# Kernel tuning notes

Hardware: AMD Instinct MI355X
Metric: run time of the kernel (lower is better)

The kernel has to match this reference:

```python
import jax, jax.numpy as jnp
import numpy as np
import math

N = 1500; E = 24000; C_IN = 16; H = 64; NUM_LAYERS = 10; RATIO = 0.9
NEG = -1e9


def setup_inputs() -> dict:
    key = jax.random.key(0)
    ks = jax.random.split(key, 40)
    it = iter(range(40))
    def nrm(shape, scale=0.1):
        return jax.random.normal(ks[next(it)], shape, dtype=jnp.float32) * scale
    src = jax.random.randint(ks[next(it)], (E,), 0, N, dtype=jnp.int32)
    off = jax.random.randint(ks[next(it)], (E,), 1, N, dtype=jnp.int32)
    dst = (src + off) % N  # no self loops in the raw edge list
    return dict(
        x=nrm((N, C_IN), 1.0),
        edge_src=src, edge_dst=dst,
        W1=nrm((C_IN, H // 2)), b1=jnp.zeros((H // 2,), jnp.float32),
        W2=nrm((H // 2, H)), b2=jnp.zeros((H,), jnp.float32),
        W3=nrm((H, H)), b3=jnp.zeros((H,), jnp.float32),
        Wrel=nrm((NUM_LAYERS - 1, H, H)), brel=jnp.zeros((NUM_LAYERS - 1, H), jnp.float32),
        Wroot=nrm((NUM_LAYERS - 1, H, H)),
        pW=nrm((4, H, H)), pb=jnp.zeros((4, H), jnp.float32),
        leW1=nrm((4, H, 1)), leb1=jnp.zeros((4, 1), jnp.float32),
        leW2=nrm((4, H, 1)),
        leW3=nrm((4, H, 1)), leb3=jnp.zeros((4, 1), jnp.float32),
        linW1=nrm((NUM_LAYERS * H, H)), linb1=jnp.zeros((H,), jnp.float32),
        linW2=nrm((H, 10)), linb2=jnp.zeros((10,), jnp.float32),
    )


def _seg_mean(vals, idx, n):
    s = jax.ops.segment_sum(vals, idx, num_segments=n)
    c = jax.ops.segment_sum(jnp.ones((idx.shape[0],), vals.dtype), idx, num_segments=n)
    return s / jnp.maximum(c, 1.0)[:, None]


def _feast(x, W, b, srcL, dstL, n):
    # FeaStConv with heads=1: softmax over a single head == 1 -> mean of lin(x_j) + bias
    return _seg_mean((x @ W)[srcL], dstL, n) + b


def _gconv_sparse(x, src, dst, Wr, br, Wo, n):
    return _seg_mean(x[src], dst, n) @ Wr + br + x @ Wo


def _gconv_dense(x, A, Wr, br, Wo):
    # mean aggregation: divide weighted sum by count of (nonzero) in-edges
    Mf = (A != 0).astype(x.dtype)
    agg = (A.T @ x) / jnp.maximum(Mf.sum(0), 1.0)[:, None]
    return agg @ Wr + br + x @ Wo


def _topk_pool(xc, fitness, ratio):
    k = int(math.ceil(ratio * xc.shape[0]))
    fit_k, perm = jax.lax.top_k(fitness, k)
    return xc[perm] * fit_k[:, None], perm


def _asap_sparse(x, src, dst, pW, pb, leW1, leb1, leW2, leW3, leb3):
    n = x.shape[0]
    ar = jnp.arange(n, dtype=src.dtype)
    srcL = jnp.concatenate([src, ar])  # add remaining self loops (weight 1)
    dstL = jnp.concatenate([dst, ar])
    xq = jax.ops.segment_max(x[srcL], dstL, num_segments=n) @ pW + pb
    s = jax.nn.leaky_relu(jnp.sum(xq[dstL] * x[srcL], -1), 0.2)
    m = jax.ops.segment_max(s, dstL, num_segments=n)
    e = jnp.exp(s - m[dstL])
    score = e / jax.ops.segment_sum(e, dstL, num_segments=n)[dstL]
    xc = jax.ops.segment_sum(x[srcL] * score[:, None], dstL, num_segments=n)
    # LEConv fitness score (edge weight = 1)
    a = xc @ leW1 + leb1
    b = xc @ leW2
    agg = jax.ops.segment_sum(a[srcL] - b[dstL], dstL, num_segments=n)
    fitness = jax.nn.sigmoid((agg + xc @ leW3 + leb3)[:, 0])
    x_new, perm = _topk_pool(xc, fitness, RATIO)
    S = jnp.zeros((n, n), x.dtype).at[srcL, dstL].add(score)
    A = jnp.zeros((n, n), x.dtype).at[srcL, dstL].add(1.0)
    Sp = S[:, perm]
    A_new = Sp.T @ A @ Sp
    k = A_new.shape[0]
    return x_new, A_new * (1.0 - jnp.eye(k, dtype=x.dtype))  # remove diag


def _asap_dense(x, A, pW, pb, leW1, leb1, leW2, leW3, leb3):
    n = x.shape[0]
    A = A + jnp.diag((jnp.diag(A) == 0).astype(A.dtype))  # add remaining self loops
    M = A != 0
    Mf = M.astype(x.dtype)
    xq = jnp.max(jnp.where(M[:, :, None], x[:, None, :], NEG), axis=0) @ pW + pb  # [n,H]
    Sc = jnp.where(M, jax.nn.leaky_relu(x @ xq.T, 0.2), NEG)  # [j,i]
    m = Sc.max(0)
    e = jnp.where(M, jnp.exp(Sc - m), 0.0)
    score = e / e.sum(0)
    xc = score.T @ x
    a = xc @ leW1 + leb1
    b = xc @ leW2
    agg = Mf.T @ a - Mf.sum(0)[:, None] * b
    fitness = jax.nn.sigmoid((agg + xc @ leW3 + leb3)[:, 0])
    x_new, perm = _topk_pool(xc, fitness, RATIO)
    Sp = score[:, perm]
    A_new = Sp.T @ A @ Sp
    k = A_new.shape[0]
    return x_new, A_new * (1.0 - jnp.eye(k, dtype=x.dtype))


def _forward(x, edge_src, edge_dst, W1, b1, W2, b2, W3, b3, Wrel, brel, Wroot,
             pW, pb, leW1, leb1, leW2, leW3, leb3, linW1, linb1, linW2, linb2):
    n = x.shape[0]
    ar = jnp.arange(n, dtype=edge_src.dtype)
    srcL = jnp.concatenate([edge_src, ar])  # FeaStConv add_self_loops=True
    dstL = jnp.concatenate([edge_dst, ar])
    x = jax.nn.elu(_feast(x, W1, b1, srcL, dstL, n))
    x = jax.nn.elu(_feast(x, W2, b2, srcL, dstL, n))
    x = jax.nn.elu(_feast(x, W3, b3, srcL, dstL, n))
    xs = [x.mean(0, keepdims=True)]  # single graph -> global_mean_pool == mean
    A = None
    for i in range(NUM_LAYERS - 1):
        if A is None:
            x = jax.nn.relu(_gconv_sparse(x, edge_src, edge_dst, Wrel[i], brel[i], Wroot[i], x.shape[0]))
        else:
            x = jax.nn.relu(_gconv_dense(x, A, Wrel[i], brel[i], Wroot[i]))
        xs.append(x.mean(0, keepdims=True))
        if i % 2 == 0 and i < NUM_LAYERS - 2:
            p = i // 2
            args = (pW[p], pb[p], leW1[p], leb1[p], leW2[p], leW3[p], leb3[p])
            if A is None:
                x, A = _asap_sparse(x, edge_src, edge_dst, *args)
            else:
                x, A = _asap_dense(x, A, *args)
    h = jnp.concatenate(xs, axis=-1)  # [1, NUM_LAYERS*H] jumping-knowledge cat
    h = jax.nn.relu(h @ linW1 + linb1)
    return jax.nn.log_softmax(h @ linW2 + linb2, axis=-1)


def reference(x, edge_src, edge_dst, W1, b1, W2, b2, W3, b3, Wrel, brel, Wroot,
              pW, pb, leW1, leb1, leW2, leW3, leb3, linW1, linb1, linW2, linb2):
    return _forward(x, edge_src, edge_dst, W1, b1, W2, b2, W3, b3, Wrel, brel, Wroot,
                    pW, pb, leW1, leb1, leW2, leW3, leb3, linW1, linb1, linW2, linb2)
```

## Files before the change

### kernel.cpp

```cpp
#include <hip/hip_runtime.h>
#include <math.h>

#define NEGV -1000000000.0f

typedef short short8 __attribute__((ext_vector_type(8)));
typedef float floatx4 __attribute__((ext_vector_type(4)));

__device__ __forceinline__ float sigm(float x){ return 1.0f/(1.0f+expf(-x)); }
__device__ __forceinline__ void edge_sd(int e,const int* src,const int* dst,int E,int& s,int& d){
  if(e<E){ s=src[e]; d=dst[e]; } else { s=e-E; d=s; }
}
__device__ __forceinline__ ushort bf16rn(float x){
  unsigned u = __float_as_uint(x);
  unsigned r = (u + 0x7fffu + ((u>>16)&1u)) >> 16;
  return (ushort)r;
}
__device__ __forceinline__ float bf16f(ushort h){ return __uint_as_float(((unsigned)h)<<16); }

__global__ void k_zero(float* __restrict__ p, size_t n){
  size_t i = (size_t)blockIdx.x*256 + threadIdx.x;
  if (i < n) p[i] = 0.0f;
}
__global__ void k_fillm1(int* __restrict__ p, int n){
  int i = blockIdx.x*256 + threadIdx.x;
  if (i < n) p[i] = -1;
}
__global__ void k_ipos(const int* __restrict__ perm, int* __restrict__ ipos, int kk){
  int p = blockIdx.x*256 + threadIdx.x;
  if (p < kk) ipos[perm[p]] = p;
}
__global__ void k_prep2(const int* __restrict__ rowD,const int* __restrict__ eidD,
                        const float* __restrict__ scE,int2* __restrict__ Mt,int L2,int kk){
  int p = blockIdx.x*256+threadIdx.x; if(p>=L2) return;
  Mt[p] = make_int2(rowD[p]*kk, __float_as_int(scE[eidD[p]]));
}

__global__ void k_split3(const float* __restrict__ src,int R,int Cs,int ld,
                         ushort* __restrict__ dst,int Cp,int bmode){
  int idx = blockIdx.x*256+threadIdx.x;
  if (idx >= R*Cp) return;
  int r = idx / Cp, c = idx - r*Cp;
  float x = (c < Cs) ? src[(size_t)r*ld + c] : 0.0f;
  ushort h = bf16rn(x);
  ushort l = bf16rn(x - bf16f(h));
  size_t base = (size_t)r*(3*Cp) + c;
  dst[base]        = h;
  dst[base + Cp]   = bmode ? l : h;
  dst[base + 2*Cp] = bmode ? h : l;
}
__global__ void k_split3_Tdual(const float* __restrict__ src,int Rs,int Cs,int ld,
                               const int* __restrict__ gperm,const float* __restrict__ cscale,
                               const float* __restrict__ emax,
                               ushort* __restrict__ dstA,ushort* __restrict__ dstB,
                               ushort* __restrict__ dstCpad,int Kp){
  __shared__ float t[32][33];
  int tx = threadIdx.x & 31, ty = threadIdx.x >> 5;
  int kb = blockIdx.y*32, xb = blockIdx.x*32;
  int x = xb + tx;
  int gx = (x < Cs) ? gperm[x] : 0;
#pragma unroll
  for (int i=0;i<4;i++){
    int k = kb + ty + i*8;
    t[ty+i*8][tx] = (k < Rs && x < Cs) ? src[(size_t)k*ld + gx] : 0.0f;
  }
  __syncthreads();
  const int K3 = 3*Kp;
#pragma unroll
  for (int i=0;i<4;i++){
    int xo = xb + ty + i*8, ko = kb + tx;
    if (xo < Cs){
      float v = 0.0f;
      if (ko < Rs){
        int g = gperm[xo];
        v = expf(t[tx][ty+i*8] - emax[g]) * cscale[g];
      }
      ushort h = bf16rn(v);
      ushort l = bf16rn(v - bf16f(h));
      size_t base = (size_t)xo*K3 + ko;
      dstA[base] = h; dstA[base+Kp] = h; dstA[base+2*Kp] = l;
      dstB[base] = h; dstB[base+Kp] = l; dstB[base+2*Kp] = h;
      if (ko >= Rs){ dstCpad[base]=0; dstCpad[base+Kp]=0; dstCpad[base+2*Kp]=0; }
    }
  }
}

template<int EPI>
__global__ __launch_bounds__(256) void k_gemm_mfma(
    const ushort* __restrict__ A, const ushort* __restrict__ B,
    float* __restrict__ C, int ldc, int M, int N, int K3,
    const float* __restrict__ mask, int ldm)
{
  __shared__ ushort As[2][64][72];
  __shared__ ushort Bs[2][64][72];
  const int tid = threadIdx.x;
  const int m0 = blockIdx.y*64, n0 = blockIdx.x*64;
  const int w = tid>>6, lane = tid&63;
  const int lo4 = lane&15, quad = lane>>4;
  const int sr = tid>>2, sseg = tid&3;

  floatx4 acc[4];
#pragma unroll
  for(int c=0;c<4;c++){ acc[c][0]=0.f; acc[c][1]=0.f; acc[c][2]=0.f; acc[c][3]=0.f; }

  const size_t arow = (size_t)(m0+sr)*K3;
  const size_t brow = (size_t)(n0+sr)*K3;
  const bool aval = (m0+sr) < M;
  const bool bval = (n0+sr) < N;

  uint4 av0 = make_uint4(0,0,0,0), av1 = make_uint4(0,0,0,0);
  uint4 bv0 = make_uint4(0,0,0,0), bv1 = make_uint4(0,0,0,0);
  if (aval){ av0 = *(const uint4*)(A + arow + sseg*8);
             av1 = *(const uint4*)(A + arow + 32 + sseg*8); }
  if (bval){ bv0 = *(const uint4*)(B + brow + sseg*8);
             bv1 = *(const uint4*)(B + brow + 32 + sseg*8); }
  *(uint4*)&As[0][sr][sseg*8] = av0; *(uint4*)&As[0][sr][32+sseg*8] = av1;
  *(uint4*)&Bs[0][sr][sseg*8] = bv0; *(uint4*)&Bs[0][sr][32+sseg*8] = bv1;
  __syncthreads();

  const int T = K3 >> 6;
  for (int i=0;i<T;i++){
    const int cb = i & 1;
    if (i+1 < T){
      const int k0 = (i+1)<<6;
      av0 = make_uint4(0,0,0,0); av1 = make_uint4(0,0,0,0);
      bv0 = make_uint4(0,0,0,0); bv1 = make_uint4(0,0,0,0);
      if (aval){ av0 = *(const uint4*)(A + arow + k0 + sseg*8);
                 av1 = *(const uint4*)(A + arow + k0 + 32 + sseg*8); }
      if (bval){ bv0 = *(const uint4*)(B + brow + k0 + sseg*8);
                 bv1 = *(const uint4*)(B + brow + k0 + 32 + sseg*8); }
    }
    short8 af0 = *(const short8*)&As[cb][16*w + lo4][quad*8];
    short8 af1 = *(const short8*)&As[cb][16*w + lo4][32+quad*8];
#pragma unroll
    for (int c=0;c<4;c++){
      short8 bf0 = *(const short8*)&Bs[cb][16*c + lo4][quad*8];
      acc[c] = __builtin_amdgcn_mfma_f32_16x16x32_bf16(af0, bf0, acc[c], 0, 0, 0);
      short8 bf1 = *(const short8*)&Bs[cb][16*c + lo4][32+quad*8];
      acc[c] = __builtin_amdgcn_mfma_f32_16x16x32_bf16(af1, bf1, acc[c], 0, 0, 0);
    }
    if (i+1 < T){
      __syncthreads();
      *(uint4*)&As[1-cb][sr][sseg*8] = av0; *(uint4*)&As[1-cb][sr][32+sseg*8] = av1;
      *(uint4*)&Bs[1-cb][sr][sseg*8] = bv0; *(uint4*)&Bs[1-cb][sr][32+sseg*8] = bv1;
      __syncthreads();
    }
  }

#pragma unroll
  for (int c=0;c<4;c++){
    const int gn = n0 + 16*c + lo4;
#pragma unroll
    for (int r=0;r<4;r++){
      const int gm = m0 + 16*w + quad*4 + r;
      if (gm < M && gn < N){
        float v = acc[c][r];
        if (EPI==1) v = (mask[(size_t)gm*ldm+gn] != 0.0f || gm==gn) ? (v > 0.0f ? v : 0.2f*v) : NEGV;
        C[(size_t)gm*ldc+gn] = v;
      }
    }
  }
}

__global__ __launch_bounds__(256) void k_gemm_pp(
    const ushort* __restrict__ A, const ushort* __restrict__ B,
    float* __restrict__ P0, float* __restrict__ P1, int ldp,
    int M, int N, int K3, int kchunk)
{
  __shared__ ushort As[2][64][72];
  __shared__ ushort Bs[2][64][72];
  const int tid = threadIdx.x;
  const int m0 = blockIdx.y*64, n0 = blockIdx.x*64;
  const int w = tid>>6, lane = tid&63;
  const int lo4 = lane&15, quad = lane>>4;
  const int l6 = tid & 63;
  const int rw = (((l6>>2)&3)<<1) | ((l6>>4)&1) | (((l6>>5)&1)<<3);
  const int sr = ((tid>>6)<<4) | rw;
  const int sseg = tid&3;

  const int z = blockIdx.z;
  float* __restrict__ P = z ? P1 : P0;
  const int kbeg = z * kchunk;
  int klen = K3 - kbeg; if (klen > kchunk) klen = kchunk;
  const int T = klen >> 6;

  floatx4 acc[4];
#pragma unroll
  for(int c=0;c<4;c++){ acc[c][0]=0.f; acc[c][1]=0.f; acc[c][2]=0.f; acc[c][3]=0.f; }

  const size_t arow = (size_t)(m0+sr)*K3 + kbeg;
  const size_t brow = (size_t)(n0+sr)*K3 + kbeg;
  const bool aval = (m0+sr) < M;
  const bool bval = (n0+sr) < N;

  uint4 av0 = make_uint4(0,0,0,0), av1 = make_uint4(0,0,0,0);
  uint4 bv0 = make_uint4(0,0,0,0), bv1 = make_uint4(0,0,0,0);
  if (aval){ av0 = *(const uint4*)(A + arow + sseg*8);
             av1 = *(const uint4*)(A + arow + 32 + sseg*8); }
  if (bval){ bv0 = *(const uint4*)(B + brow + sseg*8);
             bv1 = *(const uint4*)(B + brow + 32 + sseg*8); }
  *(uint4*)&As[0][sr][sseg*8] = av0; *(uint4*)&As[0][sr][32+sseg*8] = av1;
  *(uint4*)&Bs[0][sr][sseg*8] = bv0; *(uint4*)&Bs[0][sr][32+sseg*8] = bv1;
  __syncthreads();

  for (int i=0;i<T;i++){
    const int cb = i & 1;
    if (i+1 < T){
      const int k0 = (i+1)<<6;
      av0 = make_uint4(0,0,0,0); av1 = make_uint4(0,0,0,0);
      bv0 = make_uint4(0,0,0,0); bv1 = make_uint4(0,0,0,0);
      if (aval){ av0 = *(const uint4*)(A + arow + k0 + sseg*8);
                 av1 = *(const uint4*)(A + arow + k0 + 32 + sseg*8); }
      if (bval){ bv0 = *(const uint4*)(B + brow + k0 + sseg*8);
                 bv1 = *(const uint4*)(B + brow + k0 + 32 + sseg*8); }
    }
    short8 af0 = *(const short8*)&As[cb][16*w + lo4][quad*8];
    short8 af1 = *(const short8*)&As[cb][16*w + lo4][32+quad*8];
#pragma unroll
    for (int c=0;c<4;c++){
      short8 bf0 = *(const short8*)&Bs[cb][16*c + lo4][quad*8];
      acc[c] = __builtin_amdgcn_mfma_f32_16x16x32_bf16(af0, bf0, acc[c], 0, 0, 0);
      short8 bf1 = *(const short8*)&Bs[cb][16*c + lo4][32+quad*8];
      acc[c] = __builtin_amdgcn_mfma_f32_16x16x32_bf16(af1, bf1, acc[c], 0, 0, 0);
    }
    if (i+1 < T){
      __syncthreads();
      *(uint4*)&As[1-cb][sr][sseg*8] = av0; *(uint4*)&As[1-cb][sr][32+sseg*8] = av1;
      *(uint4*)&Bs[1-cb][sr][sseg*8] = bv0; *(uint4*)&Bs[1-cb][sr][32+sseg*8] = bv1;
      __syncthreads();
    }
  }

#pragma unroll
  for (int c=0;c<4;c++){
    const int gn = n0 + 16*c + lo4;
#pragma unroll
    for (int r=0;r<4;r++){
      const int gm = m0 + 16*w + quad*4 + r;
      if (gm < M && gn < N) P[(size_t)gm*ldp+gn] = acc[c][r];
    }
  }
}

__global__ __launch_bounds__(256) void k_red_tb(
    const float* __restrict__ P0,const float* __restrict__ P1,int ldp,
    const ushort* __restrict__ Bb, ushort* __restrict__ Cb,
    int M,int N,int Kp)
{
  __shared__ float t[32][33];
  const int tx = threadIdx.x & 31, ty = threadIdx.x >> 5;
  const int mb = blockIdx.y*32, nb = blockIdx.x*32;
  const int n = nb + tx;
#pragma unroll
  for (int i=0;i<4;i++){
    int m = mb + ty + i*8;
    float v = 0.0f;
    if (m < M && n < N){ size_t o = (size_t)m*ldp + n; v = P0[o] + P1[o]; }
    t[ty+i*8][tx] = v;
  }
  __syncthreads();
  const int K3o = 3*Kp;
#pragma unroll
  for (int i=0;i<4;i++){
    int no = nb + ty + i*8, mo = mb + tx;
    if (no < N && mo < M){
      size_t base = (size_t)no*K3o + mo;
      float sp = bf16f(Bb[base]) + bf16f(Bb[base+Kp]);
      float v = t[tx][ty+i*8] + sp;
      ushort h = bf16rn(v), l = bf16rn(v - bf16f(h));
      Cb[base] = h; Cb[base+Kp] = l; Cb[base+2*Kp] = h;
    }
  }
}

__global__ void k_red_diag(const float* __restrict__ P0,const float* __restrict__ P1,
                           float* __restrict__ C,int kk){
  int idx = blockIdx.x*256+threadIdx.x;
  if (idx >= kk*kk) return;
  int u = idx/kk, v = idx - u*kk;
  C[idx] = (u==v) ? 0.0f : (P0[idx] + P1[idx]);
}

template<bool MAXM, bool COUNT, bool EXPM, bool SELF>
__global__ __launch_bounds__(256) void k_skinny(
    const float* __restrict__ A, int lda,
    const float* __restrict__ X,
    const float* __restrict__ mcol,
    float* __restrict__ P, int* __restrict__ cntp,
    int M, int K, int kchunk)
{
  __shared__ float As[16][68];
  __shared__ float Xs[16][68];
  const int tid = threadIdx.x;
  const int m0 = blockIdx.y * 64;
  const int tmb = (tid & 15) * 4, tnb = (tid >> 4) * 4;
  float acc[4][4];
  int cacc[4] = {0,0,0,0};
#pragma unroll
  for (int i=0;i<4;i++)
#pragma unroll
    for (int j=0;j<4;j++) acc[i][j] = MAXM ? NEGV : 0.0f;

  const int kstart = blockIdx.z * kchunk;
  int kend = kstart + kchunk; if (kend > K) kend = K;
  const int ml = tid & 63, tb = tid >> 6;
  const bool mvalid = (m0 + ml) < M;
  float mc = 0.0f;
  if (EXPM && mvalid) mc = mcol[m0 + ml];

  for (int k0 = kstart; k0 < kend; k0 += 16) {
#pragma unroll
    for (int s=0;s<4;s++) {
      const int tk = tb + s*4;
      float va = 0.0f, vx = 0.0f;
      if ((k0+tk) < K) {
        if (mvalid){
          va = A[(size_t)(k0+tk)*lda + m0 + ml];
          if (EXPM) va = expf(va - mc);
        }
        vx = X[(size_t)(k0+tk)*64 + ml];
      }
      As[tk][ml] = va;
      Xs[tk][ml] = vx;
    }
    __syncthreads();
#pragma unroll
    for (int kk=0; kk<16; kk++) {
      const float4 a4 = *(const float4*)&As[kk][tmb];
      const float4 b4 = *(const float4*)&Xs[kk][tnb];
      const float av[4] = {a4.x,a4.y,a4.z,a4.w};
      const float bv[4] = {b4.x,b4.y,b4.z,b4.w};
#pragma unroll
      for (int i=0;i<4;i++){
        if (COUNT) cacc[i] += (av[i] != 0.0f) ? 1 : 0;
#pragma unroll
        for (int j=0;j<4;j++) {
          if (MAXM) acc[i][j] = fmaxf(acc[i][j], av[i] != 0.0f ? bv[j] : NEGV);
          else      acc[i][j] = fmaf(av[i], bv[j], acc[i][j]);
        }
      }
    }
    __syncthreads();
  }

  const size_t slab = (size_t)blockIdx.z * M * 64;
#pragma unroll
  for (int i=0;i<4;i++){
    const int m = m0 + tmb + i;
    if (m < M){
#pragma unroll
      for (int j=0;j<4;j++){
        float v = acc[i][j];
        if (SELF) v = fmaxf(v, X[(size_t)m*64 + tnb + j]);
        P[slab + (size_t)m*64 + tnb + j] = v;
      }
    }
  }
  if (COUNT && tnb == 0){
#pragma unroll
    for (int i=0;i<4;i++){
      const int m = m0 + tmb + i;
      if (m < M) cntp[blockIdx.z*M + m] = cacc[i];
    }
  }
}

__global__ __launch_bounds__(256) void k_poolq(
    const float* __restrict__ SEGP,const int* __restrict__ cntp8,int Z,
    const float* __restrict__ pWp,const float* __restrict__ pbp,
    const float* __restrict__ X,
    ushort* __restrict__ dstA,ushort* __restrict__ dstB,
    float* __restrict__ cntP,int n)
{
  __shared__ float xq[4][65];
  const int tid = threadIdx.x;
  const int r = tid>>6, j = tid&63;
  const int i = blockIdx.x*4 + r;
  float v = NEGV;
  if (i < n){
    for(int z=0;z<Z;z++) v = fmaxf(v, SEGP[(size_t)z*n*64 + (size_t)i*64 + j]);
    if (j == 0){
      int c=1; for(int z=0;z<Z;z++) c += cntp8[z*n+i];
      cntP[i] = (float)c;
    }
  }
  xq[r][j] = v;
  __syncthreads();
  if (i < n){
    float s = pbp[j];
    for(int q=0;q<64;q++) s = fmaf(xq[r][q], pWp[q*64+j], s);
    size_t base = (size_t)i*192 + j;
    ushort h = bf16rn(s), l = bf16rn(s - bf16f(h));
    dstB[base] = h; dstB[base+64] = l; dstB[base+128] = h;
    float x = X[(size_t)i*64 + j];
    h = bf16rn(x); l = bf16rn(x - bf16f(h));
    dstA[base] = h; dstA[base+64] = h; dstA[base+128] = l;
  }
}

__global__ __launch_bounds__(256) void k_gconv_fuse(
    const float* __restrict__ SEGP,const int* __restrict__ cntp8,int Z,
    const float* __restrict__ Wrel,const float* __restrict__ brel,
    const float* __restrict__ X,const float* __restrict__ Wroot,
    float* __restrict__ XN,int n,float* __restrict__ meanacc,float inv_n)
{
  __shared__ float agg_s[4][65];
  __shared__ float xrow[4][65];
  __shared__ float cnt_s[4];
  const int tid = threadIdx.x;
  const int r = tid>>6, j = tid&63;
  const int i = blockIdx.x*4 + r;
  float a = 0.0f;
  if (i < n){
    for(int z=0;z<Z;z++) a += SEGP[(size_t)z*n*64 + (size_t)i*64 + j];
    xrow[r][j] = X[(size_t)i*64 + j];
    if (j == 0){
      int c=0; for(int z=0;z<Z;z++) c += cntp8[z*n+i];
      cnt_s[r] = (float)(c>1?c:1);
    }
  }
  agg_s[r][j] = a;
  __syncthreads();
  float v = 0.0f;
  if (i < n){
    float acc=0.0f, rt=0.0f;
    for(int q=0;q<64;q++){
      acc = fmaf(agg_s[r][q], Wrel[q*64+j], acc);
      rt  = fmaf(xrow[r][q],  Wroot[q*64+j], rt);
    }
    v = fmaxf(acc/cnt_s[r] + brel[j] + rt, 0.0f);
    XN[(size_t)i*64 + j] = v;
  }
  __syncthreads();
  agg_s[r][j] = v;
  __syncthreads();
  if (r == 0) atomicAdd(&meanacc[j], (agg_s[0][j]+agg_s[1][j]+agg_s[2][j]+agg_s[3][j])*inv_n);
}

__global__ __launch_bounds__(256) void k_smax_fused(const float* __restrict__ S,int n,
                                                    float* __restrict__ mcol,float* __restrict__ invd){
  __shared__ float red[16][17];
  const int jc = threadIdx.x & 15, rg = threadIdx.x >> 4;
  const int j = blockIdx.x*16 + jc;
  float m = -3.0e38f;
  if (j < n)
    for(int i=rg;i<n;i+=16) m = fmaxf(m, S[(size_t)i*n+j]);
  red[rg][jc] = m;
  __syncthreads();
  for(int s=8;s>0;s>>=1){
    if(rg<s) red[rg][jc] = fmaxf(red[rg][jc], red[rg+s][jc]);
    __syncthreads();
  }
  const float mc = red[0][jc];
  __syncthreads();
  float sum = 0.0f;
  if (j < n)
    for(int i=rg;i<n;i+=16) sum += expf(S[(size_t)i*n+j]-mc);
  red[rg][jc] = sum;
  __syncthreads();
  for(int s=8;s>0;s>>=1){
    if(rg<s) red[rg][jc] += red[rg+s][jc];
    __syncthreads();
  }
  if(rg==0 && j<n){ mcol[j]=mc; invd[j]=1.0f/red[0][jc]; }
}

__global__ __launch_bounds__(256) void k_xcabc_dense(
    const float* __restrict__ SEGP,int Z,const float* __restrict__ invd,
    float* __restrict__ XC,
    const float* __restrict__ w1,const float* bb1,const float* __restrict__ w2,
    const float* __restrict__ w3,const float* bb3,
    float* aN,float* bN,float* cN,int* pcnt,int n)
{
  __shared__ float xc[4][65];
  const int tid = threadIdx.x;
  const int r = tid>>6, j = tid&63;
  const int i = blockIdx.x*4 + r;
  if (blockIdx.x==0 && tid==0) *pcnt = 0;
  float v = 0.0f;
  if (i < n){
    for(int z=0;z<Z;z++) v += SEGP[(size_t)z*n*64 + (size_t)i*64 + j];
    v *= invd[i];
    XC[(size_t)i*64+j] = v;
  }
  xc[r][j] = v;
  __syncthreads();
  if (i < n && j < 3){
    float s = (j==0)?bb1[0]:((j==2)?bb3[0]:0.0f);
    const float* w = (j==0)?w1:((j==1)?w2:w3);
    for(int q=0;q<64;q++) s = fmaf(xc[r][q], w[q], s);
    if(j==0) aN[i]=s; else if(j==1) bN[i]=s; else cN[i]=s;
  }
}

__global__ void k_aggcol(const float* __restrict__ A,const float* __restrict__ aN,
                         float* __restrict__ aggp,int n){
  int idx = blockIdx.x*256+threadIdx.x; if(idx>=n*16) return;
  int j = idx % n, c = idx / n;
  int i0 = (int)(((long long)n*c)/16), i1 = (int)(((long long)n*(c+1))/16);
  float s = 0.0f;
  for(int i=i0;i<i1;i++) if(A[(size_t)i*n + j] != 0.0f) s += aN[i];
  aggp[c*n + j] = s;
}

template<int MODE>
__global__ __launch_bounds__(256) void k_rank_fused(
    const float* __restrict__ fit_in,
    const float* __restrict__ aggp,const float* __restrict__ cntP,
    const float* __restrict__ aN,const float* __restrict__ bN,const float* __restrict__ cN,
    const float* __restrict__ XC,float* __restrict__ XN,
    int n,int k,int* pcnt,int* perm)
{
  __shared__ float fs[1504];
  const int tid = threadIdx.x;
  for(int u=tid; u<n; u+=256){
    float f;
    if (MODE==0) f = fit_in[u];
    else {
      float a = aN[u];
      for(int c=0;c<16;c++) a += aggp[c*n+u];
      f = sigm(a - cntP[u]*bN[u] + cN[u]);
    }
    fs[u] = f;
  }
  __syncthreads();
  const int v = blockIdx.x*256+tid; if(v>=n) return;
  const float fv = fs[v]; int r = 0;
  for(int u=0;u<n;u++){ float fu = fs[u]; r += (fu > fv || (fu == fv && u < v)) ? 1 : 0; }
  if (r < k){
    int p = atomicAdd(pcnt,1);
    perm[p] = v;
    const float* src = XC + (size_t)v*64;
    float* d = XN + (size_t)p*64;
    for(int h=0;h<64;h++) d[h] = src[h]*fv;
  }
}

__global__ void k_deg(const int* __restrict__ src,const int* __restrict__ dst,int* indeg,int* outdeg,int E){
  int e = blockIdx.x*256+threadIdx.x; if(e>=E) return;
  atomicAdd(&indeg[dst[e]],1); atomicAdd(&outdeg[src[e]],1);
}
__global__ __launch_bounds__(256) void k_prefix2(const int* __restrict__ indeg,const int* __restrict__ outdeg,
                          int* offD,int* curD,int* offS,int* curS,int n){
  __shared__ int ds[1504];
  const int* dsrc = blockIdx.y ? outdeg : indeg;
  for(int u=threadIdx.x; u<n; u+=256) ds[u] = dsrc[u];
  __syncthreads();
  int t = blockIdx.x*256+threadIdx.x; if(t>n) return;
  int s = 0;
  for(int u=0;u<t;u++) s += ds[u]+1;
  if (blockIdx.y){ offS[t]=s; if(t<n) curS[t]=s; }
  else           { offD[t]=s; if(t<n) curD[t]=s; }
}
__global__ void k_csr_fill2(const int* src,const int* dst,
                            int* curS,int* colS,int* eidS,
                            int* curD,int* rowD,int* eidD,int E,int n){
  int e = blockIdx.x*256+threadIdx.x; if(e>=E+n) return;
  int s,d; edge_sd(e,src,dst,E,s,d);
  int p = atomicAdd(&curS[s],1); colS[p]=d; eidS[p]=e;
  int q = atomicAdd(&curD[d],1); rowD[q]=s; eidD[q]=e;
}

__global__ void k_mm_small(const float* __restrict__ A,const float* __restrict__ W,
                           const float* __restrict__ b,float* __restrict__ C,
                           int M,int K,int Np,int act){
  int idx = blockIdx.x*256+threadIdx.x; if(idx>=M*Np) return;
  int m = idx/Np, j = idx - m*Np;
  float s = b ? b[j] : 0.0f;
  const float* a = A + (size_t)m*K;
  for(int q=0;q<K;q++) s = fmaf(a[q], W[(size_t)q*Np + j], s);
  if(act==1) s = fmaxf(s, 0.0f);
  C[idx] = s;
}

__global__ void k_feast_gf(const float* __restrict__ Y,const int* __restrict__ offD,
                           const int* __restrict__ rowD,
                           const float* __restrict__ b,float* X,int n,int H,
                           float* __restrict__ meanacc,float inv_n){
  __shared__ float ms[4][64];
  int idx = blockIdx.x*256+threadIdx.x;
  float v = 0.0f;
  if(idx<n*H){
    int i = idx/H, h = idx - i*H;
    int p0 = offD[i], p1 = offD[i+1];
    float s = 0.0f;
    for(int p=p0;p<p1;p++) s += Y[(size_t)rowD[p]*H + h];
    float t = s/(float)(p1-p0) + b[h];
    v = t > 0.0f ? t : (expf(t)-1.0f);
    X[idx] = v;
  }
  if(meanacc){
    int r = threadIdx.x>>6, j = threadIdx.x&63;
    ms[r][j] = (idx<n*H) ? v : 0.0f;
    __syncthreads();
    if(r==0) atomicAdd(&meanacc[j], (ms[0][j]+ms[1][j]+ms[2][j]+ms[3][j])*inv_n);
  }
}

__global__ __launch_bounds__(256) void k_gconv_sparse_f(
    const float* __restrict__ X,const int* __restrict__ offD,const int* __restrict__ rowD,
    const int* __restrict__ eidD,int E,
    const float* __restrict__ Wrel,const float* __restrict__ brel,
    const float* __restrict__ Wroot,
    float* __restrict__ XN,int n,float* __restrict__ meanacc,float inv_n)
{
  __shared__ float agg_s[4][65];
  __shared__ float xrow[4][65];
  __shared__ float cnt_s[4];
  const int tid = threadIdx.x;
  const int r = tid>>6, j = tid&63;
  const int i = blockIdx.x*4 + r;
  float a = 0.0f;
  if (i < n){
    int p0 = offD[i], p1 = offD[i+1], c = 0;
    for(int p=p0;p<p1;p++){
      if (eidD[p] < E){ a += X[(size_t)rowD[p]*64 + j]; c++; }
    }
    xrow[r][j] = X[(size_t)i*64 + j];
    if (j == 0) cnt_s[r] = (float)(c>1?c:1);
  }
  agg_s[r][j] = a;
  __syncthreads();
  float v = 0.0f;
  if (i < n){
    float acc=0.0f, rt=0.0f;
    for(int q=0;q<64;q++){
      acc = fmaf(agg_s[r][q], Wrel[q*64+j], acc);
      rt  = fmaf(xrow[r][q],  Wroot[q*64+j], rt);
    }
    v = fmaxf(acc/cnt_s[r] + brel[j] + rt, 0.0f);
    XN[(size_t)i*64 + j] = v;
  }
  __syncthreads();
  agg_s[r][j] = v;
  __syncthreads();
  if (r == 0) atomicAdd(&meanacc[j], (agg_s[0][j]+agg_s[1][j]+agg_s[2][j]+agg_s[3][j])*inv_n);
}

__global__ __launch_bounds__(256) void k_xqmaxq(
    const float* __restrict__ X,const int* __restrict__ offD,const int* __restrict__ rowD,
    const float* __restrict__ pWp,const float* __restrict__ pbp,
    float* __restrict__ XQ2,int n)
{
  __shared__ float xq[4][65];
  const int tid = threadIdx.x;
  const int r = tid>>6, j = tid&63;
  const int i = blockIdx.x*4 + r;
  float v = -3.0e38f;
  if (i < n){
    int p0 = offD[i], p1 = offD[i+1];
    for(int p=p0;p<p1;p++) v = fmaxf(v, X[(size_t)rowD[p]*64 + j]);
  }
  xq[r][j] = v;
  __syncthreads();
  if (i < n){
    float s = pbp[j];
    for(int q=0;q<64;q++) s = fmaf(xq[r][q], pWp[q*64+j], s);
    XQ2[(size_t)i*64+j] = s;
  }
}

__global__ void k_edge_score(const int* __restrict__ src,const int* __restrict__ dst,
                             const float* __restrict__ XQ2,const float* __restrict__ X,
                             float* sE,int E,int n){
  int e = blockIdx.x*256+threadIdx.x; if(e>=E+n) return;
  int s,d; edge_sd(e,src,dst,E,s,d);
  const float* q = XQ2 + (size_t)d*64;
  const float* x = X + (size_t)s*64;
  float acc = 0.0f;
  for(int h=0;h<64;h++) acc = fmaf(q[h], x[h], acc);
  sE[e] = acc > 0.0f ? acc : 0.2f*acc;
}

__global__ void k_dstsoft(const int* __restrict__ offD,const int* __restrict__ eidD,
                          const float* __restrict__ sE,float* __restrict__ scE,int n){
  int i = blockIdx.x*256+threadIdx.x; if(i>=n) return;
  int p0 = offD[i], p1 = offD[i+1];
  float m = -3.0e38f;
  for(int p=p0;p<p1;p++) m = fmaxf(m, sE[eidD[p]]);
  float d = 0.0f;
  for(int p=p0;p<p1;p++) d += expf(sE[eidD[p]]-m);
  float inv = 1.0f/d;
  for(int p=p0;p<p1;p++){ int e = eidD[p]; scE[e] = expf(sE[e]-m)*inv; }
}

__global__ __launch_bounds__(256) void k_xcabc0(
    const int* __restrict__ offD,const int* __restrict__ rowD,const int* __restrict__ eidD,
    const float* __restrict__ scE,const float* __restrict__ X,
    float* __restrict__ XC,
    const float* __restrict__ w1,const float* bb1,const float* __restrict__ w2,
    const float* __restrict__ w3,const float* bb3,
    float* aN,float* bN,float* cN,int* pcnt,int n)
{
  __shared__ float xc[4][65];
  const int tid = threadIdx.x;
  const int r = tid>>6, j = tid&63;
  const int i = blockIdx.x*4 + r;
  if (blockIdx.x==0 && tid==0) *pcnt = 0;
  float v = 0.0f;
  if (i < n){
    int p0 = offD[i], p1 = offD[i+1];
    for(int p=p0;p<p1;p++) v += scE[eidD[p]] * X[(size_t)rowD[p]*64 + j];
    XC[(size_t)i*64+j] = v;
  }
  xc[r][j] = v;
  __syncthreads();
  if (i < n && j < 3){
    float s = (j==0)?bb1[0]:((j==2)?bb3[0]:0.0f);
    const float* w = (j==0)?w1:((j==1)?w2:w3);
    for(int q=0;q<64;q++) s = fmaf(xc[r][q], w[q], s);
    if(j==0) aN[i]=s; else if(j==1) bN[i]=s; else cN[i]=s;
  }
}

__global__ void k_aggfit0(const int* __restrict__ offD,const int* __restrict__ rowD,
                          const float* aN,const float* bN,const float* cN,
                          float* fit,int n){
  int i = blockIdx.x*256+threadIdx.x; if(i>=n) return;
  int p0 = offD[i], p1 = offD[i+1];
  float s = 0.0f;
  for(int p=p0;p<p1;p++) s += aN[rowD[p]];
  fit[i] = sigm(s - (float)(p1-p0)*bN[i] + cN[i]);
}

__global__ void k_stage1p(const int* src,const int* dst,const int* __restrict__ offS,
                          const int* __restrict__ colS,const int* __restrict__ eidS,
                          const float* __restrict__ scE,const int* __restrict__ ipos,
                          float* Rp,int E,int n,int kk){
  int e = blockIdx.x*256+threadIdx.x; if(e>=E+n) return;
  int i,j; edge_sd(e,src,dst,E,i,j);
  int p0 = offS[j], p1 = offS[j+1];
  float* Ri = Rp + (size_t)i*kk;
  for(int p=p0;p<p1;p++){
    int ip = ipos[colS[p]];
    if (ip >= 0) atomicAdd(&Ri[ip], scE[eidS[p]]);
  }
}
__global__ __launch_bounds__(256) void k_stage2x(
    const int* __restrict__ perm,const int* __restrict__ offD,
    const int2* __restrict__ Mt,
    const float* __restrict__ Rp,float* A,int k,int vw,int cbn){
  const int bid = blockIdx.x;
  const int slice = bid & 7;
  const int rest = bid >> 3;
  const int cb = rest % cbn;
  const int ub = rest / cbn;
  const int u = ub*4 + (threadIdx.x>>6);
  if (u >= k) return;
  const int vbase = slice*vw;
  int vend = vbase + vw; if (vend > k) vend = k;
  const int v = vbase + cb*64 + (threadIdx.x&63);
  const bool vok = v < vend;
  const int vs = vok ? v : vbase;
  const int d = perm[u];
  float acc = 0.0f;
  int p = offD[d];
  const int p1 = offD[d+1];
  for(; p+4 <= p1; p += 4){
    const int2 m0 = Mt[p];
    const int2 m1 = Mt[p+1];
    const int2 m2 = Mt[p+2];
    const int2 m3 = Mt[p+3];
    const float r0 = Rp[m0.x + vs];
    const float r1 = Rp[m1.x + vs];
    const float r2 = Rp[m2.x + vs];
    const float r3 = Rp[m3.x + vs];
    acc = fmaf(__int_as_float(m0.y), r0, acc);
    acc = fmaf(__int_as_float(m1.y), r1, acc);
    acc = fmaf(__int_as_float(m2.y), r2, acc);
    acc = fmaf(__int_as_float(m3.y), r3, acc);
  }
  for(; p < p1; ++p){
    const int2 m = Mt[p];
    acc = fmaf(__int_as_float(m.y), Rp[m.x + vs], acc);
  }
  if (vok) A[(size_t)u*k + v] = (u==v) ? 0.0f : acc;
}

__global__ void k_head2(const float* __restrict__ xs,const float* __restrict__ W1,
                        const float* __restrict__ b1,const float* __restrict__ W2,
                        const float* __restrict__ b2,float* out){
  __shared__ float h2[64];
  __shared__ float lg[10];
  int t = threadIdx.x;
  float s = b1[t];
  for(int q=0;q<640;q++) s = fmaf(xs[q], W1[q*64+t], s);
  h2[t] = fmaxf(s, 0.0f);
  __syncthreads();
  if(t < 10){
    float s2 = b2[t];
    for(int k=0;k<64;k++) s2 = fmaf(h2[k], W2[k*10+t], s2);
    lg[t] = s2;
  }
  __syncthreads();
  if(t == 0){
    float mx = lg[0];
    for(int i=1;i<10;i++) mx = fmaxf(mx, lg[i]);
    float se = 0.0f;
    for(int i=0;i<10;i++) se += expf(lg[i]-mx);
    float lse = mx + logf(se);
    for(int i=0;i<10;i++) out[i] = lg[i]-lse;
  }
}

extern "C" void kernel_launch(void* const* d_in, const int* in_sizes, int n_in,
                              void* d_out, int out_size, void* d_ws, size_t ws_size,
                              hipStream_t stream) {
  const int N0 = 1500, E = 24000, Z = 16, L = E + N0;
  const float* x0   = (const float*)d_in[0];
  const int* esrc   = (const int*)d_in[1];
  const int* edst   = (const int*)d_in[2];
  const float* W1   = (const float*)d_in[3];  const float* b1   = (const float*)d_in[4];
  const float* W2   = (const float*)d_in[5];  const float* b2   = (const float*)d_in[6];
  const float* W3   = (const float*)d_in[7];  const float* b3   = (const float*)d_in[8];
  const float* Wrel = (const float*)d_in[9];  const float* brel = (const float*)d_in[10];
  const float* Wroot= (const float*)d_in[11];
  const float* pW   = (const float*)d_in[12]; const float* pb   = (const float*)d_in[13];
  const float* leW1 = (const float*)d_in[14]; const float* leb1 = (const float*)d_in[15];
  const float* leW2 = (const float*)d_in[16]; const float* leW3 = (const float*)d_in[17];
  const float* leb3 = (const float*)d_in[18];
  const float* linW1= (const float*)d_in[19]; const float* linb1= (const float*)d_in[20];
  const float* linW2= (const float*)d_in[21]; const float* linb2= (const float*)d_in[22];
  float* out = (float*)d_out;

  float* ws = (float*)d_ws;
  size_t cur = 0;
  auto allocF = [&](size_t nf)->float*{ float* p = ws + cur; cur += (nf + 15) & ~(size_t)15; return p; };
  float* xs   = allocF(640);
  int* indeg  = (int*)allocF(1504);
  int* outdeg = (int*)allocF(1504);
  float* Xa  = allocF(96000); float* Xb  = allocF(96000); float* Y   = allocF(96000);
  float* XQ2 = allocF(96000); float* XC  = allocF(96000);
  float* mcol = allocF(1504); float* invd = allocF(1504);
  float* aN = allocF(1504); float* bN = allocF(1504); float* cN = allocF(1504);
  float* fit = allocF(1504); float* cntP = allocF(1504);
  int* pcnt = (int*)allocF(16);
  int* perm = (int*)allocF(1504);
  int* offD = (int*)allocF(1504); int* offS = (int*)allocF(1504);
  int* curD = (int*)allocF(1504); int* curS = (int*)allocF(1504);
  int* colS = (int*)allocF(25504); int* eidS = (int*)allocF(25504);
  int* rowD = (int*)allocF(25504); int* eidD = (int*)allocF(25504);
  float* sE = allocF(25504); float* scE = allocF(25504);
  int2* Mt  = (int2*)allocF(51008);
  int* cntp8 = (int*)allocF((size_t)Z*1504);
  float* aggp = allocF(16*1504);
  float* SEGP = allocF((size_t)Z*1504*64);
  float* Rbig = allocF((size_t)1500*1500);
  float* SCb  = Rbig;
  float* A0  = allocF((size_t)1350*1350);
  float* A1s = allocF((size_t)1350*1350);
  const size_t BFSZ = (size_t)1350*4224/2 + 32;
  ushort* Abf = (ushort*)allocF(BFSZ);
  ushort* Bbf = (ushort*)allocF(BFSZ);
  ushort* Cbf = (ushort*)allocF(BFSZ);
  ushort* Dbf = (ushort*)allocF(BFSZ);

  dim3 B256(256);
  auto G1 = [&](size_t n){ return dim3((unsigned)((n + 255) / 256)); };
  auto ZF = [&](void* p, size_t nfloats){ k_zero<<<G1(nfloats),B256,0,stream>>>((float*)p, nfloats); };
  auto kcz = [&](int K){ return (int)(((K + Z*16 - 1) / (Z*16)) * 16); };

  ZF(xs, 640 + 1504 + 1504);
  k_deg<<<G1(E),B256,0,stream>>>(esrc, edst, indeg, outdeg, E);
  k_prefix2<<<dim3((N0+256)/256,2),B256,0,stream>>>(indeg, outdeg, offD, curD, offS, curS, N0);
  k_csr_fill2<<<G1(L),B256,0,stream>>>(esrc, edst, curS, colS, eidS, curD, rowD, eidD, E, N0);

  auto feast = [&](const float* xin,int cin,const float* W,const float* bb,int hh,float* xout,float* macc){
    k_mm_small<<<G1((size_t)N0*hh),B256,0,stream>>>(xin, W, nullptr, Y, N0, cin, hh, 0);
    k_feast_gf<<<G1((size_t)N0*hh),B256,0,stream>>>(Y, offD, rowD, bb, xout, N0, hh, macc, 1.0f/N0);
  };
  feast(x0, 16, W1, b1, 32, Xa, nullptr);
  feast(Xa, 32, W2, b2, 64, Xb, nullptr);
  feast(Xb, 64, W3, b3, 64, Xa, xs + 0);
  float* X = Xa; float* XN = Xb;

  k_gconv_sparse_f<<<dim3((N0+3)/4),B256,0,stream>>>(X, offD, rowD, eidD, E, Wrel, brel, Wroot,
                                                     XN, N0, xs + 64, 1.0f/N0);
  { float* t = X; X = XN; XN = t; }

  {
    const int n = 1500, kk = 1350;
    k_xqmaxq<<<dim3((n+3)/4),B256,0,stream>>>(X, offD, rowD, pW, pb, XQ2, n);
    k_edge_score<<<G1(L),B256,0,stream>>>(esrc, edst, XQ2, X, sE, E, n);
    k_dstsoft<<<G1(n),B256,0,stream>>>(offD, eidD, sE, scE, n);
    k_prep2<<<G1(L),B256,0,stream>>>(rowD, eidD, scE, Mt, L, kk);
    k_xcabc0<<<dim3((n+3)/4),B256,0,stream>>>(offD, rowD, eidD, scE, X, XC,
                                              leW1, leb1, leW2, leW3, leb3, aN, bN, cN, pcnt, n);
    k_aggfit0<<<G1(n),B256,0,stream>>>(offD, rowD, aN, bN, cN, fit, n);
    k_rank_fused<0><<<G1(n),B256,0,stream>>>(fit, nullptr, nullptr, nullptr, nullptr, nullptr,
                                             XC, XN, n, kk, pcnt, perm);
    int* ipos = curD;
    k_fillm1<<<G1(n),B256,0,stream>>>(ipos, n);
    k_ipos<<<G1(kk),B256,0,stream>>>(perm, ipos, kk);
    ZF(Rbig, (size_t)n*kk);
    k_stage1p<<<G1(L),B256,0,stream>>>(esrc, edst, offS, colS, eidS, scE, ipos, Rbig, E, n, kk);
    {
      const int vw = (kk + 7) / 8;
      const int cbn = (vw + 63) / 64;
      const int ubn = (kk + 3) / 4;
      k_stage2x<<<dim3((unsigned)(8*cbn*ubn)),B256,0,stream>>>(perm, offD, Mt,
                                                               Rbig, A0, kk, vw, cbn);
    }
    { float* t = X; X = XN; XN = t; }
  }

  float* Acur = A0; float* Aoth = A1s;
  int nn = 1350;

  auto gconv_dense = [&](int layer){
    dim3 g(1, (nn+63)/64, Z);
    k_skinny<false,true,false,false><<<g,B256,0,stream>>>(Acur, nn, X, nullptr, SEGP, cntp8, nn, nn, kcz(nn));
    k_gconv_fuse<<<dim3((nn+3)/4),B256,0,stream>>>(SEGP, cntp8, Z,
        Wrel + (size_t)layer*4096, brel + layer*64, X, Wroot + (size_t)layer*4096,
        XN, nn, xs + (size_t)(layer+1)*64, 1.0f/nn);
    { float* t = X; X = XN; XN = t; }
  };

  auto asap_dense = [&](int kk, int p){
    {
      dim3 g(1, (nn+63)/64, Z);
      k_skinny<true,true,false,true><<<g,B256,0,stream>>>(Acur, nn, X, nullptr, SEGP, cntp8, nn, nn, kcz(nn));
    }
    k_poolq<<<dim3((nn+3)/4),B256,0,stream>>>(SEGP, cntp8, Z, pW + (size_t)p*4096, pb + p*64,
                                              X, Abf, Bbf, cntP, nn);
    {
      dim3 g((nn+63)/64, (nn+63)/64);
      k_gemm_mfma<1><<<g,B256,0,stream>>>(Abf, Bbf, SCb, nn, nn, nn, 192, Acur, nn);
    }
    k_smax_fused<<<dim3((nn+15)/16),B256,0,stream>>>(SCb, nn, mcol, invd);
    {
      dim3 g(1, (nn+63)/64, Z);
      k_skinny<false,false,true,false><<<g,B256,0,stream>>>(SCb, nn, X, mcol, SEGP, nullptr, nn, nn, kcz(nn));
    }
    k_xcabc_dense<<<dim3((nn+3)/4),B256,0,stream>>>(SEGP, Z, invd, XC,
        leW1 + p*64, leb1 + p, leW2 + p*64, leW3 + p*64, leb3 + p, aN, bN, cN, pcnt, nn);
    k_aggcol<<<G1((size_t)nn*16),B256,0,stream>>>(Acur, aN, aggp, nn);
    k_rank_fused<1><<<G1(nn),B256,0,stream>>>(nullptr, aggp, cntP, aN, bN, cN,
                                              XC, XN, nn, kk, pcnt, perm);
    const int Kp = (nn + 63) & ~63;
    const int K3 = 3*Kp;
    k_split3<<<G1((size_t)nn*Kp),B256,0,stream>>>(Acur, nn, nn, nn, Abf, Kp, 0);
    { dim3 gt((kk+31)/32, Kp/32);
      k_split3_Tdual<<<gt,B256,0,stream>>>(SCb, nn, kk, nn, perm, invd, mcol, Dbf, Bbf, Cbf, Kp); }
    const int Tk = K3 >> 6;
    const int kchunk = ((Tk + 1) >> 1) << 6;
    {
      float* PT0 = Rbig;
      float* PT1 = Aoth;
      dim3 g((kk+63)/64, (nn+63)/64, 2);
      k_gemm_pp<<<g,B256,0,stream>>>(Abf, Bbf, PT0, PT1, kk, nn, kk, K3, kchunk);
      dim3 gr((kk+31)/32, (nn+31)/32);
      k_red_tb<<<gr,B256,0,stream>>>(PT0, PT1, kk, Bbf, Cbf, nn, kk, Kp);
    }
    {
      float* PD0 = Rbig;
      float* PD1 = SEGP;
      dim3 g((kk+63)/64, (kk+63)/64, 2);
      k_gemm_pp<<<g,B256,0,stream>>>(Dbf, Cbf, PD0, PD1, kk, kk, kk, K3, kchunk);
      k_red_diag<<<G1((size_t)kk*kk),B256,0,stream>>>(PD0, PD1, Aoth, kk);
    }
    { float* t = X; X = XN; XN = t; }
    { float* t = Acur; Acur = Aoth; Aoth = t; }
    nn = kk;
  };

  gconv_dense(1);
  gconv_dense(2);
  asap_dense(1215, 1);
  gconv_dense(3);
  gconv_dense(4);
  asap_dense(1094, 2);
  gconv_dense(5);
  gconv_dense(6);
  asap_dense(985, 3);
  gconv_dense(7);
  gconv_dense(8);

  k_head2<<<1,64,0,stream>>>(xs, linW1, linb1, linW2, linb2, out);
}
```

Before: 1.424 ms.

## Parallelize top-k ranking across blocks and raise split-K factor to four

```diff
diff --git a/kernel.cpp b/kernel.cpp
--- a/kernel.cpp
+++ b/kernel.cpp
@@ -163,7 +163,8 @@
 
 __global__ __launch_bounds__(256) void k_gemm_pp(
     const ushort* __restrict__ A, const ushort* __restrict__ B,
-    float* __restrict__ P0, float* __restrict__ P1, int ldp,
+    float* __restrict__ P0, float* __restrict__ P1,
+    float* __restrict__ P2, float* __restrict__ P3, int ldp,
     int M, int N, int K3, int kchunk)
 {
   __shared__ ushort As[2][64][72];
@@ -178,9 +179,9 @@
   const int sseg = tid&3;
 
   const int z = blockIdx.z;
-  float* __restrict__ P = z ? P1 : P0;
+  float* __restrict__ P = (z==0) ? P0 : (z==1) ? P1 : (z==2) ? P2 : P3;
   const int kbeg = z * kchunk;
-  int klen = K3 - kbeg; if (klen > kchunk) klen = kchunk;
+  int klen = K3 - kbeg; if (klen > kchunk) klen = kchunk; if (klen < 0) klen = 0;
   const int T = klen >> 6;
 
   floatx4 acc[4];
@@ -242,7 +243,8 @@
 }
 
 __global__ __launch_bounds__(256) void k_red_tb(
-    const float* __restrict__ P0,const float* __restrict__ P1,int ldp,
+    const float* __restrict__ P0,const float* __restrict__ P1,
+    const float* __restrict__ P2,const float* __restrict__ P3,int ldp,
     const ushort* __restrict__ Bb, ushort* __restrict__ Cb,
     int M,int N,int Kp)
 {
@@ -254,7 +256,10 @@
   for (int i=0;i<4;i++){
     int m = mb + ty + i*8;
     float v = 0.0f;
-    if (m < M && n < N){ size_t o = (size_t)m*ldp + n; v = P0[o] + P1[o]; }
+    if (m < M && n < N){
+      size_t o = (size_t)m*ldp + n;
+      v = (P0[o] + P1[o]) + (P2[o] + P3[o]);
+    }
     t[ty+i*8][tx] = v;
   }
   __syncthreads();
@@ -273,11 +278,13 @@
 }
 
 __global__ void k_red_diag(const float* __restrict__ P0,const float* __restrict__ P1,
+                           const float* __restrict__ P2,const float* __restrict__ P3,
                            float* __restrict__ C,int kk){
   int idx = blockIdx.x*256+threadIdx.x;
   if (idx >= kk*kk) return;
   int u = idx/kk, v = idx - u*kk;
-  C[idx] = (u==v) ? 0.0f : (P0[idx] + P1[idx]);
+  float s = (P0[idx] + P1[idx]) + (P2[idx] + P3[idx]);
+  C[idx] = (u==v) ? 0.0f : s;
 }
 
 template<bool MAXM, bool COUNT, bool EXPM, bool SELF>
@@ -502,36 +509,53 @@
   aggp[c*n + j] = s;
 }
 
-template<int MODE>
-__global__ __launch_bounds__(256) void k_rank_fused(
-    const float* __restrict__ fit_in,
-    const float* __restrict__ aggp,const float* __restrict__ cntP,
-    const float* __restrict__ aN,const float* __restrict__ bN,const float* __restrict__ cN,
-    const float* __restrict__ XC,float* __restrict__ XN,
-    int n,int k,int* pcnt,int* perm)
-{
-  __shared__ float fs[1504];
-  const int tid = threadIdx.x;
-  for(int u=tid; u<n; u+=256){
-    float f;
-    if (MODE==0) f = fit_in[u];
-    else {
-      float a = aN[u];
-      for(int c=0;c<16;c++) a += aggp[c*n+u];
-      f = sigm(a - cntP[u]*bN[u] + cN[u]);
-    }
-    fs[u] = f;
-  }
-  __syncthreads();
-  const int v = blockIdx.x*256+tid; if(v>=n) return;
-  const float fv = fs[v]; int r = 0;
-  for(int u=0;u<n;u++){ float fu = fs[u]; r += (fu > fv || (fu == fv && u < v)) ? 1 : 0; }
-  if (r < k){
+__global__ void k_fit_dense(const float* __restrict__ aggp,const float* __restrict__ cntP,
+                            const float* __restrict__ aN,const float* __restrict__ bN,
+                            const float* __restrict__ cN,
+                            float* __restrict__ fit,int* __restrict__ rank,int* pcnt,int n){
+  int u = blockIdx.x*256+threadIdx.x;
+  if (blockIdx.x==0 && threadIdx.x==0) *pcnt = 0;
+  if (u >= n) return;
+  float a = aN[u];
+  for(int c=0;c<16;c++) a += aggp[c*n+u];
+  fit[u] = sigm(a - cntP[u]*bN[u] + cN[u]);
+  rank[u] = 0;
+}
+__global__ __launch_bounds__(256) void k_rank_cnt(const float* __restrict__ fit,
+                                                  int* __restrict__ rank,int n){
+  __shared__ float fsc[128];
+  const int u0 = blockIdx.y*128;
+  int u1 = u0+128; if (u1 > n) u1 = n;
+  const int cl = u1 - u0;
+  if ((int)threadIdx.x < cl) fsc[threadIdx.x] = fit[u0+threadIdx.x];
+  __syncthreads();
+  const int v = blockIdx.x*256+threadIdx.x;
+  if (v >= n) return;
+  const float fv = fit[v];
+  int r = 0;
+  for(int t=0;t<cl;t++){
+    const float fu = fsc[t];
+    const int u = u0+t;
+    r += (fu > fv || (fu == fv && u < v)) ? 1 : 0;
+  }
+  atomicAdd(&rank[v], r);
+}
+__global__ __launch_bounds__(256) void k_rank_sel(const int* __restrict__ rank,
+    const float* __restrict__ fit,const float* __restrict__ XC,float* __restrict__ XN,
+    int n,int k,int* pcnt,int* perm){
+  __shared__ int ps[4];
+  const int r = threadIdx.x>>6, h = threadIdx.x&63;
+  const int v = blockIdx.x*4 + r;
+  const bool sel = (v < n) && (rank[v] < k);
+  if (h == 0 && sel){
     int p = atomicAdd(pcnt,1);
+    ps[r] = p;
     perm[p] = v;
-    const float* src = XC + (size_t)v*64;
-    float* d = XN + (size_t)p*64;
-    for(int h=0;h<64;h++) d[h] = src[h]*fv;
+  }
+  __syncthreads();
+  if (sel){
+    const int p = ps[r];
+    XN[(size_t)p*64 + h] = XC[(size_t)v*64 + h] * fit[v];
   }
 }
 
@@ -714,12 +738,13 @@
 
 __global__ void k_aggfit0(const int* __restrict__ offD,const int* __restrict__ rowD,
                           const float* aN,const float* bN,const float* cN,
-                          float* fit,int n){
+                          float* fit,int* __restrict__ rank,int n){
   int i = blockIdx.x*256+threadIdx.x; if(i>=n) return;
   int p0 = offD[i], p1 = offD[i+1];
   float s = 0.0f;
   for(int p=p0;p<p1;p++) s += aN[rowD[p]];
   fit[i] = sigm(s - (float)(p1-p0)*bN[i] + cN[i]);
+  rank[i] = 0;
 }
 
 __global__ void k_stage1p(const int* src,const int* dst,const int* __restrict__ offS,
@@ -848,11 +873,15 @@
   float* SCb  = Rbig;
   float* A0  = allocF((size_t)1350*1350);
   float* A1s = allocF((size_t)1350*1350);
+  const size_t SLAB = 1650048;
+  float* PS2 = allocF(SLAB);
+  float* PS3 = allocF(SLAB);
   const size_t BFSZ = (size_t)1350*4224/2 + 32;
   ushort* Abf = (ushort*)allocF(BFSZ);
   ushort* Bbf = (ushort*)allocF(BFSZ);
   ushort* Cbf = (ushort*)allocF(BFSZ);
   ushort* Dbf = (ushort*)allocF(BFSZ);
+  int* rankb = indeg;
 
   dim3 B256(256);
   auto G1 = [&](size_t n){ return dim3((unsigned)((n + 255) / 256)); };
@@ -885,9 +914,9 @@
     k_prep2<<<G1(L),B256,0,stream>>>(rowD, eidD, scE, Mt, L, kk);
     k_xcabc0<<<dim3((n+3)/4),B256,0,stream>>>(offD, rowD, eidD, scE, X, XC,
                                               leW1, leb1, leW2, leW3, leb3, aN, bN, cN, pcnt, n);
-    k_aggfit0<<<G1(n),B256,0,stream>>>(offD, rowD, aN, bN, cN, fit, n);
-    k_rank_fused<0><<<G1(n),B256,0,stream>>>(fit, nullptr, nullptr, nullptr, nullptr, nullptr,
-                                             XC, XN, n, kk, pcnt, perm);
+    k_aggfit0<<<G1(n),B256,0,stream>>>(offD, rowD, aN, bN, cN, fit, rankb, n);
+    k_rank_cnt<<<dim3((n+255)/256,(n+127)/128),B256,0,stream>>>(fit, rankb, n);
+    k_rank_sel<<<dim3((n+3)/4),B256,0,stream>>>(rankb, fit, XC, XN, n, kk, pcnt, perm);
     int* ipos = curD;
     k_fillm1<<<G1(n),B256,0,stream>>>(ipos, n);
     k_ipos<<<G1(kk),B256,0,stream>>>(perm, ipos, kk);
@@ -934,29 +963,26 @@
     k_xcabc_dense<<<dim3((nn+3)/4),B256,0,stream>>>(SEGP, Z, invd, XC,
         leW1 + p*64, leb1 + p, leW2 + p*64, leW3 + p*64, leb3 + p, aN, bN, cN, pcnt, nn);
     k_aggcol<<<G1((size_t)nn*16),B256,0,stream>>>(Acur, aN, aggp, nn);
-    k_rank_fused<1><<<G1(nn),B256,0,stream>>>(nullptr, aggp, cntP, aN, bN, cN,
-                                              XC, XN, nn, kk, pcnt, perm);
+    k_fit_dense<<<G1(nn),B256,0,stream>>>(aggp, cntP, aN, bN, cN, fit, rankb, pcnt, nn);
+    k_rank_cnt<<<dim3((nn+255)/256,(nn+127)/128),B256,0,stream>>>(fit, rankb, nn);
+    k_rank_sel<<<dim3((nn+3)/4),B256,0,stream>>>(rankb, fit, XC, XN, nn, kk, pcnt, perm);
     const int Kp = (nn + 63) & ~63;
     const int K3 = 3*Kp;
     k_split3<<<G1((size_t)nn*Kp),B256,0,stream>>>(Acur, nn, nn, nn, Abf, Kp, 0);
     { dim3 gt((kk+31)/32, Kp/32);
       k_split3_Tdual<<<gt,B256,0,stream>>>(SCb, nn, kk, nn, perm, invd, mcol, Dbf, Bbf, Cbf, Kp); }
     const int Tk = K3 >> 6;
-    const int kchunk = ((Tk + 1) >> 1) << 6;
+    const int kchunk = ((Tk + 3) >> 2) << 6;
     {
-      float* PT0 = Rbig;
-      float* PT1 = Aoth;
-      dim3 g((kk+63)/64, (nn+63)/64, 2);
-      k_gemm_pp<<<g,B256,0,stream>>>(Abf, Bbf, PT0, PT1, kk, nn, kk, K3, kchunk);
+      dim3 g((kk+63)/64, (nn+63)/64, 4);
+      k_gemm_pp<<<g,B256,0,stream>>>(Abf, Bbf, Rbig, Aoth, PS2, PS3, kk, nn, kk, K3, kchunk);
       dim3 gr((kk+31)/32, (nn+31)/32);
-      k_red_tb<<<gr,B256,0,stream>>>(PT0, PT1, kk, Bbf, Cbf, nn, kk, Kp);
+      k_red_tb<<<gr,B256,0,stream>>>(Rbig, Aoth, PS2, PS3, kk, Bbf, Cbf, nn, kk, Kp);
     }
     {
-      float* PD0 = Rbig;
-      float* PD1 = SEGP;
-      dim3 g((kk+63)/64, (kk+63)/64, 2);
-      k_gemm_pp<<<g,B256,0,stream>>>(Dbf, Cbf, PD0, PD1, kk, kk, kk, K3, kchunk);
-      k_red_diag<<<G1((size_t)kk*kk),B256,0,stream>>>(PD0, PD1, Aoth, kk);
+      dim3 g((kk+63)/64, (kk+63)/64, 4);
+      k_gemm_pp<<<g,B256,0,stream>>>(Dbf, Cbf, Rbig, Aoth, PS2, PS3, kk, kk, kk, K3, kchunk);
+      k_red_diag<<<G1((size_t)kk*kk),B256,0,stream>>>(Rbig, Aoth, PS2, PS3, Aoth, kk);
     }
     { float* t = X; X = XN; XN = t; }
     { float* t = Acur; Acur = Aoth; Aoth = t; }
```

After: 1.373 ms. -3.6%, faster.
